# Kernel optimization log

Hardware: AMD Instinct MI355X
Metric: run time of the kernel (lower is better)

## Reference

```python
import jax, jax.numpy as jnp
import numpy as np

N = 100000      # nodes
DIN = 64        # input feature dim
H = 64          # hidden dim
OUT = 2         # classifier output dim
E_REL = 1600000 # edges per relation
E_Q = 1000000   # query edges to classify


def _deg_norm(idx, n, dtype):
    # D^{-1/2} with zero-degree -> 0 (DGL norm='both' semantics)
    deg = jax.ops.segment_sum(jnp.ones(idx.shape[0], dtype=dtype), idx, num_segments=n)
    return jnp.where(deg > 0, jax.lax.rsqrt(jnp.maximum(deg, 1.0)), 0.0)


def graph_conv(x, src, dst, W, b):
    # DGL GraphConv, norm='both': out = D_in^{-1/2} A D_out^{-1/2} x W + b
    n = x.shape[0]
    c_src = _deg_norm(src, n, x.dtype)   # out-degree norm on src side
    c_dst = _deg_norm(dst, n, x.dtype)   # in-degree norm on dst side
    h = x * c_src[:, None]
    agg = jax.ops.segment_sum(h[src], dst, num_segments=n)  # gather -> scatter-add
    agg = agg * c_dst[:, None]
    return agg @ W + b


def setup_inputs() -> dict:
    key = jax.random.key(0)
    ks = jax.random.split(key, 16)
    x = jax.random.normal(ks[0], (N, DIN), dtype=jnp.float32)
    src_pos = jax.random.randint(ks[1], (E_REL,), 0, N)
    dst_pos = jax.random.randint(ks[2], (E_REL,), 0, N)
    src_neg = jax.random.randint(ks[3], (E_REL,), 0, N)
    dst_neg = jax.random.randint(ks[4], (E_REL,), 0, N)
    edge_index = jax.random.randint(ks[5], (2, E_Q), 0, N)
    s_in = 1.0 / np.sqrt(DIN)
    s_h = 1.0 / np.sqrt(H)
    return {
        "x": x,
        "W0_pos": jax.random.uniform(ks[6], (DIN, H), jnp.float32, -s_in, s_in),
        "b0_pos": jnp.zeros((H,), jnp.float32),
        "W0_neg": jax.random.uniform(ks[7], (DIN, H), jnp.float32, -s_in, s_in),
        "b0_neg": jnp.zeros((H,), jnp.float32),
        "W1_pos": jax.random.uniform(ks[8], (H, H), jnp.float32, -s_h, s_h),
        "b1_pos": jnp.zeros((H,), jnp.float32),
        "W1_neg": jax.random.uniform(ks[9], (H, H), jnp.float32, -s_h, s_h),
        "b1_neg": jnp.zeros((H,), jnp.float32),
        "Wc": jax.random.uniform(ks[10], (2 * H, OUT), jnp.float32, -s_h, s_h),
        "bc": jnp.zeros((OUT,), jnp.float32),
        "src_pos": src_pos, "dst_pos": dst_pos,
        "src_neg": src_neg, "dst_neg": dst_neg,
        "edge_index": edge_index,
    }


def reference(x, W0_pos, b0_pos, W0_neg, b0_neg, W1_pos, b1_pos, W1_neg, b1_neg,
              Wc, bc, src_pos, dst_pos, src_neg, dst_neg, edge_index):
    # Layer 1: per-relation GraphConv on input feats, ReLU (HeteroGraphConv 'all' keeps per-relation streams)
    h_pos = jax.nn.relu(graph_conv(x, src_pos, dst_pos, W0_pos, b0_pos))
    h_neg = jax.nn.relu(graph_conv(x, src_neg, dst_neg, W0_neg, b0_neg))
    # Layer 2: each relation stream convolved on its own relation graph
    z_pos = jax.nn.relu(graph_conv(h_pos, src_pos, dst_pos, W1_pos, b1_pos))
    z_neg = jax.nn.relu(graph_conv(h_neg, src_neg, dst_neg, W1_neg, b1_neg))
    z = z_pos - z_neg                         # [N, H]
    src_ids, dst_ids = edge_index[0], edge_index[1]
    h_pair = jnp.concatenate([z[src_ids], z[dst_ids]], axis=1)  # [E_Q, 2H]
    logits = h_pair @ Wc + bc
    return z, jax.nn.sigmoid(logits)
```

## Files before the change

### kernel.cpp

```cpp
#include <hip/hip_runtime.h>
#include <hip/hip_fp16.h>
#include <math.h>

#define N_NODES 100000
#define DIM 64
#define E_REL 1600000
#define E_QQ 1000000

#define NBUCK 196
#define BCAP 9216
#define CHUNK_E 8192
#define P1_BLOCKS ((E_REL + CHUNK_E - 1) / CHUNK_E)

__global__ __launch_bounds__(256) void bin_edges(
    const int* __restrict__ src, const int* __restrict__ dst,
    int* __restrict__ gcur_d, int* __restrict__ gcur_s,
    unsigned* __restrict__ bin_d, unsigned* __restrict__ bin_s) {
  __shared__ int cd[NBUCK];
  __shared__ int cs[NBUCK];
  int t = threadIdx.x;
  for (int i = t; i < NBUCK; i += 256) { cd[i] = 0; cs[i] = 0; }
  __syncthreads();
  int e0 = blockIdx.x * CHUNK_E;
  int e1 = e0 + CHUNK_E;
  if (e1 > E_REL) e1 = E_REL;
  for (int e = e0 + t; e < e1; e += 256) {
    atomicAdd(&cd[dst[e] >> 9], 1);
    atomicAdd(&cs[src[e] >> 9], 1);
  }
  __syncthreads();
  for (int i = t; i < NBUCK; i += 256) {
    cd[i] = atomicAdd(&gcur_d[i], cd[i]);
    cs[i] = atomicAdd(&gcur_s[i], cs[i]);
  }
  __syncthreads();
  for (int e = e0 + t; e < e1; e += 256) {
    int s = src[e];
    int d = dst[e];
    int bd = d >> 9;
    int bs = s >> 9;
    int pd = atomicAdd(&cd[bd], 1);
    int ps = atomicAdd(&cs[bs], 1);
    if ((unsigned)pd < BCAP)
      bin_d[(size_t)bd * BCAP + pd] = (unsigned)(((d & 511) << 17) | s);
    if ((unsigned)ps < BCAP)
      bin_s[(size_t)bs * BCAP + ps] = (unsigned)s;
  }
}

__global__ __launch_bounds__(256) void build_tables(
    const unsigned* __restrict__ bin_d, const int* __restrict__ gcur_d,
    const unsigned* __restrict__ bin_s, const int* __restrict__ gcur_s,
    int* __restrict__ offs, int* __restrict__ degv, int* __restrict__ srclist,
    float* __restrict__ csrc) {
  __shared__ int cnt[512];
  __shared__ int off0[512];
  __shared__ int curv[512];
  __shared__ int ls[256];
  int t = threadIdx.x;
  if (blockIdx.x >= NBUCK) {
    int b = blockIdx.x - NBUCK;
    cnt[t] = 0;
    cnt[t + 256] = 0;
    __syncthreads();
    int n = gcur_s[b];
    if (n > BCAP) n = BCAP;
    const unsigned* be = bin_s + (size_t)b * BCAP;
    for (int i = t; i < n; i += 256) atomicAdd(&cnt[be[i] & 511], 1);
    __syncthreads();
    int node0 = b << 9;
    for (int i = t; i < 512; i += 256) {
      int node = node0 + i;
      if (node < N_NODES) {
        int d = cnt[i];
        csrc[node] = d > 0 ? rsqrtf((float)d) : 0.0f;
      }
    }
    return;
  }
  int b = blockIdx.x;
  cnt[t] = 0;
  cnt[t + 256] = 0;
  __syncthreads();
  int n = gcur_d[b];
  if (n > BCAP) n = BCAP;
  const unsigned* be = bin_d + (size_t)b * BCAP;
  for (int i = t; i < n; i += 256) atomicAdd(&cnt[be[i] >> 17], 1);
  __syncthreads();
  int c0 = cnt[2 * t], c1 = cnt[2 * t + 1];
  ls[t] = c0 + c1;
  __syncthreads();
  for (int off = 1; off < 256; off <<= 1) {
    int v = (t >= off) ? ls[t - off] : 0;
    __syncthreads();
    ls[t] += v;
    __syncthreads();
  }
  int base = ls[t] - (c0 + c1);
  off0[2 * t] = base;
  off0[2 * t + 1] = base + c0;
  curv[2 * t] = base;
  curv[2 * t + 1] = base + c0;
  __syncthreads();
  for (int i = t; i < n; i += 256) {
    unsigned p = be[i];
    int dl = p >> 17;
    int pos = atomicAdd(&curv[dl], 1);
    srclist[(size_t)b * BCAP + pos] = (int)(p & 0x1FFFF);
  }
  __syncthreads();
  int node0 = b << 9;
  for (int i = t; i < 512; i += 256) {
    int node = node0 + i;
    if (node < N_NODES) {
      offs[node] = b * BCAP + off0[i];
      degv[node] = cnt[i];
    }
  }
}

__device__ inline unsigned pack_h2(float a, float b) {
  __half2 h = __floats2half2_rn(a, b);
  return *reinterpret_cast<unsigned*>(&h);
}

__global__ __launch_bounds__(256) void gemm_in_h(
    const float* __restrict__ X, const float* __restrict__ W,
    const float* __restrict__ csrc, __half* __restrict__ Y) {
  __shared__ float Ws[64 * 64];
  for (int t = threadIdx.x; t < 64 * 64; t += 256) Ws[t] = W[t];
  __syncthreads();
  int row = blockIdx.x * 256 + threadIdx.x;
  if (row >= N_NODES) return;
  const float4* xr = (const float4*)(X + (size_t)row * 64);
  float acc[64];
#pragma unroll
  for (int j = 0; j < 64; j++) acc[j] = 0.0f;
#pragma unroll
  for (int k4 = 0; k4 < 16; k4++) {
    float4 xv = xr[k4];
    const float* w0 = &Ws[(k4 * 4 + 0) * 64];
    const float* w1 = &Ws[(k4 * 4 + 1) * 64];
    const float* w2 = &Ws[(k4 * 4 + 2) * 64];
    const float* w3 = &Ws[(k4 * 4 + 3) * 64];
#pragma unroll
    for (int j = 0; j < 64; j++)
      acc[j] += xv.x * w0[j] + xv.y * w1[j] + xv.z * w2[j] + xv.w * w3[j];
  }
  float s = csrc[row];
  uint4* yr = (uint4*)(Y + (size_t)row * 64);
#pragma unroll
  for (int j8 = 0; j8 < 8; j8++) {
    uint4 u;
    u.x = pack_h2(s * acc[j8 * 8 + 0], s * acc[j8 * 8 + 1]);
    u.y = pack_h2(s * acc[j8 * 8 + 2], s * acc[j8 * 8 + 3]);
    u.z = pack_h2(s * acc[j8 * 8 + 4], s * acc[j8 * 8 + 5]);
    u.w = pack_h2(s * acc[j8 * 8 + 6], s * acc[j8 * 8 + 7]);
    yr[j8] = u;
  }
}

__device__ inline float4 agg_quad(const __half* __restrict__ Y, int beg,
                                  int deg, const int* __restrict__ srclist,
                                  int lane, int l, int q) {
  float4 a0 = make_float4(0.f, 0.f, 0.f, 0.f);
  float4 a1 = make_float4(0.f, 0.f, 0.f, 0.f);
  const __half* Yl = Y + 4 * l;
  for (int base = 0; base < deg; base += 64) {
    int chunk = deg - base;
    if (chunk > 64) chunk = 64;
    int sv = (base + lane < deg) ? srclist[beg + base + lane] : 0;
    int nq8 = chunk & ~7;
    for (int j = 0; j < nq8; j += 8) {
      int s0 = __shfl(sv, j + q);
      int s1 = __shfl(sv, j + 4 + q);
      uint2 u0 = *(const uint2*)(Yl + (size_t)s0 * 64);
      uint2 u1 = *(const uint2*)(Yl + (size_t)s1 * 64);
      float2 f;
      f = __half22float2(*reinterpret_cast<__half2*>(&u0.x));
      a0.x += f.x; a0.y += f.y;
      f = __half22float2(*reinterpret_cast<__half2*>(&u0.y));
      a0.z += f.x; a0.w += f.y;
      f = __half22float2(*reinterpret_cast<__half2*>(&u1.x));
      a1.x += f.x; a1.y += f.y;
      f = __half22float2(*reinterpret_cast<__half2*>(&u1.y));
      a1.z += f.x; a1.w += f.y;
    }
    int j0 = nq8 + q;
    int j1 = nq8 + 4 + q;
    int s0 = __shfl(sv, j0 & 63);
    int s1 = __shfl(sv, j1 & 63);
    if (j0 < chunk) {
      uint2 u = *(const uint2*)(Yl + (size_t)s0 * 64);
      float2 f;
      f = __half22float2(*reinterpret_cast<__half2*>(&u.x));
      a0.x += f.x; a0.y += f.y;
      f = __half22float2(*reinterpret_cast<__half2*>(&u.y));
      a0.z += f.x; a0.w += f.y;
    }
    if (j1 < chunk) {
      uint2 u = *(const uint2*)(Yl + (size_t)s1 * 64);
      float2 f;
      f = __half22float2(*reinterpret_cast<__half2*>(&u.x));
      a1.x += f.x; a1.y += f.y;
      f = __half22float2(*reinterpret_cast<__half2*>(&u.y));
      a1.z += f.x; a1.w += f.y;
    }
  }
  a0.x += a1.x; a0.y += a1.y; a0.z += a1.z; a0.w += a1.w;
  a0.x += __shfl_xor(a0.x, 16); a0.y += __shfl_xor(a0.y, 16);
  a0.z += __shfl_xor(a0.z, 16); a0.w += __shfl_xor(a0.w, 16);
  a0.x += __shfl_xor(a0.x, 32); a0.y += __shfl_xor(a0.y, 32);
  a0.z += __shfl_xor(a0.z, 32); a0.w += __shfl_xor(a0.w, 32);
  return a0;
}

__global__ __launch_bounds__(256) void gather_mid(
    const __half* __restrict__ Y, const int* __restrict__ offs,
    const int* __restrict__ degv, const int* __restrict__ srclist,
    const float* __restrict__ b0, const float* __restrict__ csrc,
    const float* __restrict__ W1, __half* __restrict__ Y2) {
  __shared__ float Ws[64 * 64];
  __shared__ float hs[4][64];
  for (int t = threadIdx.x; t < 64 * 64; t += 256) Ws[t] = W1[t];
  __syncthreads();
  int wid = (blockIdx.x * 256 + threadIdx.x) >> 6;
  int lane = threadIdx.x & 63;
  int wslot = threadIdx.x >> 6;
  if (wid >= N_NODES) return;
  int l = lane & 15, q = lane >> 4;
  int beg = offs[wid];
  int deg = degv[wid];
  float4 acc = agg_quad(Y, beg, deg, srclist, lane, l, q);
  float cd = deg > 0 ? rsqrtf((float)deg) : 0.0f;
  float4 bv = ((const float4*)b0)[l];
  float4 h;
  h.x = fmaxf(acc.x * cd + bv.x, 0.0f);
  h.y = fmaxf(acc.y * cd + bv.y, 0.0f);
  h.z = fmaxf(acc.z * cd + bv.z, 0.0f);
  h.w = fmaxf(acc.w * cd + bv.w, 0.0f);
  if (lane < 16) *((float4*)&hs[wslot][4 * l]) = h;
  float acc2 = 0.0f;
#pragma unroll
  for (int k4 = 0; k4 < 16; k4++) {
    float4 hv = *((const float4*)&hs[wslot][4 * k4]);
    acc2 += hv.x * Ws[(4 * k4 + 0) * 64 + lane] +
            hv.y * Ws[(4 * k4 + 1) * 64 + lane] +
            hv.z * Ws[(4 * k4 + 2) * 64 + lane] +
            hv.w * Ws[(4 * k4 + 3) * 64 + lane];
  }
  Y2[(size_t)wid * 64 + lane] = __float2half(csrc[wid] * acc2);
}

template <int MODE>
__global__ __launch_bounds__(256) void gather_fin(
    const __half* __restrict__ Y2, const int* __restrict__ offs,
    const int* __restrict__ degv, const int* __restrict__ srclist,
    const float* __restrict__ b1, float* __restrict__ z,
    float* __restrict__ uv, const float* __restrict__ Wc) {
  __shared__ float Wcs[256];
  if (MODE == 1) {
    Wcs[threadIdx.x] = Wc[threadIdx.x];
    __syncthreads();
  }
  int wid = (blockIdx.x * 256 + threadIdx.x) >> 6;
  int lane = threadIdx.x & 63;
  if (wid >= N_NODES) return;
  int l = lane & 15, q = lane >> 4;
  int beg = offs[wid];
  int deg = degv[wid];
  float4 acc = agg_quad(Y2, beg, deg, srclist, lane, l, q);
  float cd = deg > 0 ? rsqrtf((float)deg) : 0.0f;
  float4 bv = ((const float4*)b1)[l];
  float4 v;
  v.x = fmaxf(acc.x * cd + bv.x, 0.0f);
  v.y = fmaxf(acc.y * cd + bv.y, 0.0f);
  v.z = fmaxf(acc.z * cd + bv.z, 0.0f);
  v.w = fmaxf(acc.w * cd + bv.w, 0.0f);
  float* zrow = z + (size_t)wid * 64 + 4 * l;
  if (MODE == 0) {
    if (lane < 16) *((float4*)zrow) = v;
  } else {
    float4 zo = *((const float4*)zrow);
    float4 r;
    r.x = zo.x - v.x; r.y = zo.y - v.y; r.z = zo.z - v.z; r.w = zo.w - v.w;
    if (lane < 16) *((float4*)zrow) = r;
    float pu0 = r.x * Wcs[(4 * l + 0) * 2 + 0] + r.y * Wcs[(4 * l + 1) * 2 + 0] +
                r.z * Wcs[(4 * l + 2) * 2 + 0] + r.w * Wcs[(4 * l + 3) * 2 + 0];
    float pu1 = r.x * Wcs[(4 * l + 0) * 2 + 1] + r.y * Wcs[(4 * l + 1) * 2 + 1] +
                r.z * Wcs[(4 * l + 2) * 2 + 1] + r.w * Wcs[(4 * l + 3) * 2 + 1];
    float pv0 = r.x * Wcs[(64 + 4 * l + 0) * 2 + 0] + r.y * Wcs[(64 + 4 * l + 1) * 2 + 0] +
                r.z * Wcs[(64 + 4 * l + 2) * 2 + 0] + r.w * Wcs[(64 + 4 * l + 3) * 2 + 0];
    float pv1 = r.x * Wcs[(64 + 4 * l + 0) * 2 + 1] + r.y * Wcs[(64 + 4 * l + 1) * 2 + 1] +
                r.z * Wcs[(64 + 4 * l + 2) * 2 + 1] + r.w * Wcs[(64 + 4 * l + 3) * 2 + 1];
#pragma unroll
    for (int o = 1; o < 16; o <<= 1) {
      pu0 += __shfl_xor(pu0, o);
      pu1 += __shfl_xor(pu1, o);
      pv0 += __shfl_xor(pv0, o);
      pv1 += __shfl_xor(pv1, o);
    }
    if (lane == 0) {
      float4 o4 = make_float4(pu0, pu1, pv0, pv1);
      *((float4*)(uv + (size_t)wid * 4)) = o4;
    }
  }
}

__global__ __launch_bounds__(256) void classify_kernel(
    const float* __restrict__ uv, const int* __restrict__ ei,
    const float* __restrict__ bc, float* __restrict__ out) {
  int e = blockIdx.x * 256 + threadIdx.x;
  if (e >= E_QQ) return;
  int s = ei[e];
  int d = ei[E_QQ + e];
  float4 us = *((const float4*)(uv + (size_t)s * 4));
  float4 vd = *((const float4*)(uv + (size_t)d * 4));
  float l0 = us.x + vd.z + bc[0];
  float l1 = us.y + vd.w + bc[1];
  float2 o;
  o.x = 1.0f / (1.0f + __expf(-l0));
  o.y = 1.0f / (1.0f + __expf(-l1));
  *((float2*)(out + (size_t)e * 2)) = o;
}

extern "C" void kernel_launch(void* const* d_in, const int* in_sizes, int n_in,
                              void* d_out, int out_size, void* d_ws,
                              size_t ws_size, hipStream_t stream) {
  const float* x   = (const float*)d_in[0];
  const float* W0p = (const float*)d_in[1];
  const float* b0p = (const float*)d_in[2];
  const float* W0n = (const float*)d_in[3];
  const float* b0n = (const float*)d_in[4];
  const float* W1p = (const float*)d_in[5];
  const float* b1p = (const float*)d_in[6];
  const float* W1n = (const float*)d_in[7];
  const float* b1n = (const float*)d_in[8];
  const float* Wc  = (const float*)d_in[9];
  const float* bc  = (const float*)d_in[10];
  const int* sp = (const int*)d_in[11];
  const int* dp = (const int*)d_in[12];
  const int* sn = (const int*)d_in[13];
  const int* dn = (const int*)d_in[14];
  const int* ei = (const int*)d_in[15];

  float* csrc_p = (float*)d_ws;
  float* csrc_n = csrc_p + N_NODES;
  int* offs_p = (int*)(csrc_n + N_NODES);
  int* deg_p  = offs_p + N_NODES;
  int* offs_n = deg_p + N_NODES;
  int* deg_n  = offs_n + N_NODES;
  float* uv   = (float*)(deg_n + N_NODES);
  int* gcur   = (int*)(uv + 4 * N_NODES);
  unsigned* bin_d = (unsigned*)(gcur + 2 * NBUCK + 2);
  unsigned* bin_s = bin_d + (size_t)NBUCK * BCAP;
  int* srclist = (int*)(bin_s + (size_t)NBUCK * BCAP);
  __half* A = (__half*)(srclist + (size_t)NBUCK * BCAP);
  __half* B = A + (size_t)N_NODES * 64;

  float* z     = (float*)d_out;
  float* probs = z + (size_t)N_NODES * 64;

  int* gcur_d = gcur;
  int* gcur_s = gcur + NBUCK;

  const int gemmGrid = (N_NODES + 255) / 256;
  const int aggGrid  = (N_NODES * 64 + 255) / 256;

  hipMemsetAsync(gcur, 0, 2 * NBUCK * sizeof(int), stream);
  bin_edges<<<P1_BLOCKS, 256, 0, stream>>>(sp, dp, gcur_d, gcur_s, bin_d, bin_s);
  build_tables<<<2 * NBUCK, 256, 0, stream>>>(bin_d, gcur_d, bin_s, gcur_s,
                                              offs_p, deg_p, srclist, csrc_p);
  gemm_in_h<<<gemmGrid, 256, 0, stream>>>(x, W0p, csrc_p, A);
  gather_mid<<<aggGrid, 256, 0, stream>>>(A, offs_p, deg_p, srclist, b0p,
                                          csrc_p, W1p, B);
  gather_fin<0><<<aggGrid, 256, 0, stream>>>(B, offs_p, deg_p, srclist, b1p, z,
                                             uv, Wc);

  hipMemsetAsync(gcur, 0, 2 * NBUCK * sizeof(int), stream);
  bin_edges<<<P1_BLOCKS, 256, 0, stream>>>(sn, dn, gcur_d, gcur_s, bin_d, bin_s);
  build_tables<<<2 * NBUCK, 256, 0, stream>>>(bin_d, gcur_d, bin_s, gcur_s,
                                              offs_n, deg_n, srclist, csrc_n);
  gemm_in_h<<<gemmGrid, 256, 0, stream>>>(x, W0n, csrc_n, A);
  gather_mid<<<aggGrid, 256, 0, stream>>>(A, offs_n, deg_n, srclist, b0n,
                                          csrc_n, W1n, B);
  gather_fin<1><<<aggGrid, 256, 0, stream>>>(B, offs_n, deg_n, srclist, b1n, z,
                                             uv, Wc);

  classify_kernel<<<(E_QQ + 255) / 256, 256, 0, stream>>>(uv, ei, bc, probs);
}
```

Measured before the change: 627.7 us.

## Split features into 16-wide column planes and gather per plane with persistent blocks

Feature matrices are stored as four column-chunk planes of 16 halfs each, and the gather runs once per plane so each plane's working set (about 3.2 MB) stays cache-resident during the random-access gathers. The mid-layer matmul is pulled out of the gather into its own kernel, and the final uv projection moves into a separate kernel. This cuts cache misses on random row gathers, at the cost of re-reading the srclist four times and adding extra kernel launches and an extra pass over intermediate tensors.

```diff
diff --git a/kernel.cpp b/kernel.cpp
--- a/kernel.cpp
+++ b/kernel.cpp
@@ -11,6 +11,9 @@
 #define BCAP 9216
 #define CHUNK_E 8192
 #define P1_BLOCKS ((E_REL + CHUNK_E - 1) / CHUNK_E)
+#define NBLK_N 1563
+#define NCH 16
+#define N16 ((size_t)N_NODES * NCH)
 
 __global__ __launch_bounds__(256) void bin_edges(
     const int* __restrict__ src, const int* __restrict__ dst,
@@ -148,163 +151,167 @@
       acc[j] += xv.x * w0[j] + xv.y * w1[j] + xv.z * w2[j] + xv.w * w3[j];
   }
   float s = csrc[row];
-  uint4* yr = (uint4*)(Y + (size_t)row * 64);
-#pragma unroll
-  for (int j8 = 0; j8 < 8; j8++) {
-    uint4 u;
-    u.x = pack_h2(s * acc[j8 * 8 + 0], s * acc[j8 * 8 + 1]);
-    u.y = pack_h2(s * acc[j8 * 8 + 2], s * acc[j8 * 8 + 3]);
-    u.z = pack_h2(s * acc[j8 * 8 + 4], s * acc[j8 * 8 + 5]);
-    u.w = pack_h2(s * acc[j8 * 8 + 6], s * acc[j8 * 8 + 7]);
-    yr[j8] = u;
-  }
-}
-
-__device__ inline float4 agg_quad(const __half* __restrict__ Y, int beg,
-                                  int deg, const int* __restrict__ srclist,
-                                  int lane, int l, int q) {
-  float4 a0 = make_float4(0.f, 0.f, 0.f, 0.f);
-  float4 a1 = make_float4(0.f, 0.f, 0.f, 0.f);
-  const __half* Yl = Y + 4 * l;
-  for (int base = 0; base < deg; base += 64) {
-    int chunk = deg - base;
-    if (chunk > 64) chunk = 64;
-    int sv = (base + lane < deg) ? srclist[beg + base + lane] : 0;
-    int nq8 = chunk & ~7;
-    for (int j = 0; j < nq8; j += 8) {
-      int s0 = __shfl(sv, j + q);
-      int s1 = __shfl(sv, j + 4 + q);
-      uint2 u0 = *(const uint2*)(Yl + (size_t)s0 * 64);
-      uint2 u1 = *(const uint2*)(Yl + (size_t)s1 * 64);
-      float2 f;
-      f = __half22float2(*reinterpret_cast<__half2*>(&u0.x));
-      a0.x += f.x; a0.y += f.y;
-      f = __half22float2(*reinterpret_cast<__half2*>(&u0.y));
-      a0.z += f.x; a0.w += f.y;
-      f = __half22float2(*reinterpret_cast<__half2*>(&u1.x));
-      a1.x += f.x; a1.y += f.y;
-      f = __half22float2(*reinterpret_cast<__half2*>(&u1.y));
-      a1.z += f.x; a1.w += f.y;
-    }
-    int j0 = nq8 + q;
-    int j1 = nq8 + 4 + q;
-    int s0 = __shfl(sv, j0 & 63);
-    int s1 = __shfl(sv, j1 & 63);
-    if (j0 < chunk) {
-      uint2 u = *(const uint2*)(Yl + (size_t)s0 * 64);
-      float2 f;
-      f = __half22float2(*reinterpret_cast<__half2*>(&u.x));
-      a0.x += f.x; a0.y += f.y;
-      f = __half22float2(*reinterpret_cast<__half2*>(&u.y));
-      a0.z += f.x; a0.w += f.y;
-    }
-    if (j1 < chunk) {
-      uint2 u = *(const uint2*)(Yl + (size_t)s1 * 64);
-      float2 f;
-      f = __half22float2(*reinterpret_cast<__half2*>(&u.x));
-      a1.x += f.x; a1.y += f.y;
-      f = __half22float2(*reinterpret_cast<__half2*>(&u.y));
-      a1.z += f.x; a1.w += f.y;
-    }
-  }
-  a0.x += a1.x; a0.y += a1.y; a0.z += a1.z; a0.w += a1.w;
-  a0.x += __shfl_xor(a0.x, 16); a0.y += __shfl_xor(a0.y, 16);
-  a0.z += __shfl_xor(a0.z, 16); a0.w += __shfl_xor(a0.w, 16);
-  a0.x += __shfl_xor(a0.x, 32); a0.y += __shfl_xor(a0.y, 32);
-  a0.z += __shfl_xor(a0.z, 32); a0.w += __shfl_xor(a0.w, 32);
-  return a0;
-}
-
-__global__ __launch_bounds__(256) void gather_mid(
-    const __half* __restrict__ Y, const int* __restrict__ offs,
+#pragma unroll
+  for (int c = 0; c < 4; c++) {
+    uint4* yc = (uint4*)(Y + (size_t)c * N16 + (size_t)row * NCH);
+#pragma unroll
+    for (int h = 0; h < 2; h++) {
+      int f = c * 16 + h * 8;
+      uint4 u;
+      u.x = pack_h2(s * acc[f + 0], s * acc[f + 1]);
+      u.y = pack_h2(s * acc[f + 2], s * acc[f + 3]);
+      u.z = pack_h2(s * acc[f + 4], s * acc[f + 5]);
+      u.w = pack_h2(s * acc[f + 6], s * acc[f + 7]);
+      yc[h] = u;
+    }
+  }
+}
+
+__global__ __launch_bounds__(256) void gemm_mid_h(
+    const __half* __restrict__ X, const float* __restrict__ W,
+    const float* __restrict__ csrc, __half* __restrict__ Y) {
+  __shared__ float Ws[64 * 64];
+  for (int t = threadIdx.x; t < 64 * 64; t += 256) Ws[t] = W[t];
+  __syncthreads();
+  int row = blockIdx.x * 256 + threadIdx.x;
+  if (row >= N_NODES) return;
+  float acc[64];
+#pragma unroll
+  for (int j = 0; j < 64; j++) acc[j] = 0.0f;
+#pragma unroll
+  for (int c = 0; c < 4; c++) {
+    const uint4* xr = (const uint4*)(X + (size_t)c * N16 + (size_t)row * NCH);
+#pragma unroll
+    for (int h = 0; h < 2; h++) {
+      uint4 u = xr[h];
+      float2 f0 = __half22float2(*(__half2*)&u.x);
+      float2 f1 = __half22float2(*(__half2*)&u.y);
+      float2 f2 = __half22float2(*(__half2*)&u.z);
+      float2 f3 = __half22float2(*(__half2*)&u.w);
+      const float* w = &Ws[(c * 16 + h * 8) * 64];
+#pragma unroll
+      for (int j = 0; j < 64; j++)
+        acc[j] += f0.x * w[0 * 64 + j] + f0.y * w[1 * 64 + j] +
+                  f1.x * w[2 * 64 + j] + f1.y * w[3 * 64 + j] +
+                  f2.x * w[4 * 64 + j] + f2.y * w[5 * 64 + j] +
+                  f3.x * w[6 * 64 + j] + f3.y * w[7 * 64 + j];
+    }
+  }
+  float s = csrc[row];
+#pragma unroll
+  for (int c = 0; c < 4; c++) {
+    uint4* yc = (uint4*)(Y + (size_t)c * N16 + (size_t)row * NCH);
+#pragma unroll
+    for (int h = 0; h < 2; h++) {
+      int f = c * 16 + h * 8;
+      uint4 u;
+      u.x = pack_h2(s * acc[f + 0], s * acc[f + 1]);
+      u.y = pack_h2(s * acc[f + 2], s * acc[f + 3]);
+      u.z = pack_h2(s * acc[f + 4], s * acc[f + 5]);
+      u.w = pack_h2(s * acc[f + 6], s * acc[f + 7]);
+      yc[h] = u;
+    }
+  }
+}
+
+template <int PHASE>
+__global__ __launch_bounds__(256) void gather_split(
+    const __half* __restrict__ Yc, const int* __restrict__ offs,
     const int* __restrict__ degv, const int* __restrict__ srclist,
-    const float* __restrict__ b0, const float* __restrict__ csrc,
-    const float* __restrict__ W1, __half* __restrict__ Y2) {
-  __shared__ float Ws[64 * 64];
-  __shared__ float hs[4][64];
-  for (int t = threadIdx.x; t < 64 * 64; t += 256) Ws[t] = W1[t];
-  __syncthreads();
-  int wid = (blockIdx.x * 256 + threadIdx.x) >> 6;
+    const float* __restrict__ bias, __half* __restrict__ Hout,
+    float* __restrict__ z) {
+  int p = blockIdx.x / NBLK_N;
+  int nb = blockIdx.x - p * NBLK_N;
   int lane = threadIdx.x & 63;
   int wslot = threadIdx.x >> 6;
-  if (wid >= N_NODES) return;
-  int l = lane & 15, q = lane >> 4;
-  int beg = offs[wid];
-  int deg = degv[wid];
-  float4 acc = agg_quad(Y, beg, deg, srclist, lane, l, q);
-  float cd = deg > 0 ? rsqrtf((float)deg) : 0.0f;
-  float4 bv = ((const float4*)b0)[l];
-  float4 h;
-  h.x = fmaxf(acc.x * cd + bv.x, 0.0f);
-  h.y = fmaxf(acc.y * cd + bv.y, 0.0f);
-  h.z = fmaxf(acc.z * cd + bv.z, 0.0f);
-  h.w = fmaxf(acc.w * cd + bv.w, 0.0f);
-  if (lane < 16) *((float4*)&hs[wslot][4 * l]) = h;
-  float acc2 = 0.0f;
-#pragma unroll
-  for (int k4 = 0; k4 < 16; k4++) {
-    float4 hv = *((const float4*)&hs[wslot][4 * k4]);
-    acc2 += hv.x * Ws[(4 * k4 + 0) * 64 + lane] +
-            hv.y * Ws[(4 * k4 + 1) * 64 + lane] +
-            hv.z * Ws[(4 * k4 + 2) * 64 + lane] +
-            hv.w * Ws[(4 * k4 + 3) * 64 + lane];
-  }
-  Y2[(size_t)wid * 64 + lane] = __float2half(csrc[wid] * acc2);
-}
-
-template <int MODE>
-__global__ __launch_bounds__(256) void gather_fin(
-    const __half* __restrict__ Y2, const int* __restrict__ offs,
-    const int* __restrict__ degv, const int* __restrict__ srclist,
-    const float* __restrict__ b1, float* __restrict__ z,
-    float* __restrict__ uv, const float* __restrict__ Wc) {
-  __shared__ float Wcs[256];
-  if (MODE == 1) {
-    Wcs[threadIdx.x] = Wc[threadIdx.x];
-    __syncthreads();
-  }
+  int g = lane >> 2;
+  int c = lane & 3;
+  const __half* Yp = Yc + (size_t)p * N16 + 4 * c;
+  float4 bv = ((const float4*)bias)[p * 4 + c];
+  for (int wid = nb * 4 + wslot; wid < N_NODES; wid += NBLK_N * 4) {
+    int beg = offs[wid];
+    int deg = degv[wid];
+    float4 a0 = make_float4(0.f, 0.f, 0.f, 0.f);
+    float4 a1 = make_float4(0.f, 0.f, 0.f, 0.f);
+    for (int base = 0; base < deg; base += 64) {
+      int chunk = deg - base;
+      if (chunk > 64) chunk = 64;
+      int sv = (base + lane < deg) ? srclist[beg + base + lane] : 0;
+      for (int k = 0; k < chunk; k += 32) {
+        int j0 = k + g;
+        int j1 = k + 16 + g;
+        int s0 = __shfl(sv, j0 & 63);
+        int s1 = __shfl(sv, j1 & 63);
+        if (j0 < chunk) {
+          uint2 u = *(const uint2*)(Yp + (size_t)s0 * NCH);
+          float2 f0 = __half22float2(*(__half2*)&u.x);
+          float2 f1 = __half22float2(*(__half2*)&u.y);
+          a0.x += f0.x; a0.y += f0.y; a0.z += f1.x; a0.w += f1.y;
+        }
+        if (j1 < chunk) {
+          uint2 u = *(const uint2*)(Yp + (size_t)s1 * NCH);
+          float2 f0 = __half22float2(*(__half2*)&u.x);
+          float2 f1 = __half22float2(*(__half2*)&u.y);
+          a1.x += f0.x; a1.y += f0.y; a1.z += f1.x; a1.w += f1.y;
+        }
+      }
+    }
+    a0.x += a1.x; a0.y += a1.y; a0.z += a1.z; a0.w += a1.w;
+#pragma unroll
+    for (int o = 4; o < 64; o <<= 1) {
+      a0.x += __shfl_xor(a0.x, o);
+      a0.y += __shfl_xor(a0.y, o);
+      a0.z += __shfl_xor(a0.z, o);
+      a0.w += __shfl_xor(a0.w, o);
+    }
+    float cd = deg > 0 ? rsqrtf((float)deg) : 0.0f;
+    float4 v;
+    v.x = fmaxf(a0.x * cd + bv.x, 0.0f);
+    v.y = fmaxf(a0.y * cd + bv.y, 0.0f);
+    v.z = fmaxf(a0.z * cd + bv.z, 0.0f);
+    v.w = fmaxf(a0.w * cd + bv.w, 0.0f);
+    if (PHASE == 0) {
+      if (g == 0) {
+        uint2 u;
+        u.x = pack_h2(v.x, v.y);
+        u.y = pack_h2(v.z, v.w);
+        *(uint2*)(Hout + (size_t)p * N16 + (size_t)wid * NCH + 4 * c) = u;
+      }
+    } else if (PHASE == 1) {
+      if (g == 0)
+        *(float4*)(z + (size_t)wid * 64 + p * 16 + 4 * c) = v;
+    } else {
+      if (g == 0) {
+        float4* zp = (float4*)(z + (size_t)wid * 64 + p * 16 + 4 * c);
+        float4 zo = *zp;
+        zo.x -= v.x; zo.y -= v.y; zo.z -= v.z; zo.w -= v.w;
+        *zp = zo;
+      }
+    }
+  }
+}
+
+__global__ __launch_bounds__(256) void uv_kernel(
+    const float* __restrict__ z, const float* __restrict__ Wc,
+    float* __restrict__ uv) {
   int wid = (blockIdx.x * 256 + threadIdx.x) >> 6;
   int lane = threadIdx.x & 63;
   if (wid >= N_NODES) return;
-  int l = lane & 15, q = lane >> 4;
-  int beg = offs[wid];
-  int deg = degv[wid];
-  float4 acc = agg_quad(Y2, beg, deg, srclist, lane, l, q);
-  float cd = deg > 0 ? rsqrtf((float)deg) : 0.0f;
-  float4 bv = ((const float4*)b1)[l];
-  float4 v;
-  v.x = fmaxf(acc.x * cd + bv.x, 0.0f);
-  v.y = fmaxf(acc.y * cd + bv.y, 0.0f);
-  v.z = fmaxf(acc.z * cd + bv.z, 0.0f);
-  v.w = fmaxf(acc.w * cd + bv.w, 0.0f);
-  float* zrow = z + (size_t)wid * 64 + 4 * l;
-  if (MODE == 0) {
-    if (lane < 16) *((float4*)zrow) = v;
-  } else {
-    float4 zo = *((const float4*)zrow);
-    float4 r;
-    r.x = zo.x - v.x; r.y = zo.y - v.y; r.z = zo.z - v.z; r.w = zo.w - v.w;
-    if (lane < 16) *((float4*)zrow) = r;
-    float pu0 = r.x * Wcs[(4 * l + 0) * 2 + 0] + r.y * Wcs[(4 * l + 1) * 2 + 0] +
-                r.z * Wcs[(4 * l + 2) * 2 + 0] + r.w * Wcs[(4 * l + 3) * 2 + 0];
-    float pu1 = r.x * Wcs[(4 * l + 0) * 2 + 1] + r.y * Wcs[(4 * l + 1) * 2 + 1] +
-                r.z * Wcs[(4 * l + 2) * 2 + 1] + r.w * Wcs[(4 * l + 3) * 2 + 1];
-    float pv0 = r.x * Wcs[(64 + 4 * l + 0) * 2 + 0] + r.y * Wcs[(64 + 4 * l + 1) * 2 + 0] +
-                r.z * Wcs[(64 + 4 * l + 2) * 2 + 0] + r.w * Wcs[(64 + 4 * l + 3) * 2 + 0];
-    float pv1 = r.x * Wcs[(64 + 4 * l + 0) * 2 + 1] + r.y * Wcs[(64 + 4 * l + 1) * 2 + 1] +
-                r.z * Wcs[(64 + 4 * l + 2) * 2 + 1] + r.w * Wcs[(64 + 4 * l + 3) * 2 + 1];
-#pragma unroll
-    for (int o = 1; o < 16; o <<= 1) {
-      pu0 += __shfl_xor(pu0, o);
-      pu1 += __shfl_xor(pu1, o);
-      pv0 += __shfl_xor(pv0, o);
-      pv1 += __shfl_xor(pv1, o);
-    }
-    if (lane == 0) {
-      float4 o4 = make_float4(pu0, pu1, pv0, pv1);
-      *((float4*)(uv + (size_t)wid * 4)) = o4;
-    }
-  }
+  float w0 = Wc[lane * 2 + 0];
+  float w1 = Wc[lane * 2 + 1];
+  float w2 = Wc[(64 + lane) * 2 + 0];
+  float w3 = Wc[(64 + lane) * 2 + 1];
+  float r = z[(size_t)wid * 64 + lane];
+  float p0 = r * w0, p1 = r * w1, p2 = r * w2, p3 = r * w3;
+#pragma unroll
+  for (int o = 1; o < 64; o <<= 1) {
+    p0 += __shfl_xor(p0, o);
+    p1 += __shfl_xor(p1, o);
+    p2 += __shfl_xor(p2, o);
+    p3 += __shfl_xor(p3, o);
+  }
+  if (lane == 0)
+    *(float4*)(uv + (size_t)wid * 4) = make_float4(p0, p1, p2, p3);
 }
 
 __global__ __launch_bounds__(256) void classify_kernel(
@@ -344,14 +351,11 @@
   const int* dn = (const int*)d_in[14];
   const int* ei = (const int*)d_in[15];
 
-  float* csrc_p = (float*)d_ws;
-  float* csrc_n = csrc_p + N_NODES;
-  int* offs_p = (int*)(csrc_n + N_NODES);
-  int* deg_p  = offs_p + N_NODES;
-  int* offs_n = deg_p + N_NODES;
-  int* deg_n  = offs_n + N_NODES;
-  float* uv   = (float*)(deg_n + N_NODES);
-  int* gcur   = (int*)(uv + 4 * N_NODES);
+  float* csrc = (float*)d_ws;
+  int* degv = (int*)(csrc + N_NODES);
+  int* offs = degv + N_NODES;
+  float* uv = (float*)(offs + N_NODES);
+  int* gcur = (int*)(uv + 4 * N_NODES);
   unsigned* bin_d = (unsigned*)(gcur + 2 * NBUCK + 2);
   unsigned* bin_s = bin_d + (size_t)NBUCK * BCAP;
   int* srclist = (int*)(bin_s + (size_t)NBUCK * BCAP);
@@ -365,27 +369,30 @@
   int* gcur_s = gcur + NBUCK;
 
   const int gemmGrid = (N_NODES + 255) / 256;
-  const int aggGrid  = (N_NODES * 64 + 255) / 256;
+  const int gathGrid = 4 * NBLK_N;
 
   hipMemsetAsync(gcur, 0, 2 * NBUCK * sizeof(int), stream);
   bin_edges<<<P1_BLOCKS, 256, 0, stream>>>(sp, dp, gcur_d, gcur_s, bin_d, bin_s);
   build_tables<<<2 * NBUCK, 256, 0, stream>>>(bin_d, gcur_d, bin_s, gcur_s,
-                                              offs_p, deg_p, srclist, csrc_p);
-  gemm_in_h<<<gemmGrid, 256, 0, stream>>>(x, W0p, csrc_p, A);
-  gather_mid<<<aggGrid, 256, 0, stream>>>(A, offs_p, deg_p, srclist, b0p,
-                                          csrc_p, W1p, B);
-  gather_fin<0><<<aggGrid, 256, 0, stream>>>(B, offs_p, deg_p, srclist, b1p, z,
-                                             uv, Wc);
+                                              offs, degv, srclist, csrc);
+  gemm_in_h<<<gemmGrid, 256, 0, stream>>>(x, W0p, csrc, A);
+  gather_split<0><<<gathGrid, 256, 0, stream>>>(A, offs, degv, srclist, b0p, B,
+                                                nullptr);
+  gemm_mid_h<<<gemmGrid, 256, 0, stream>>>(B, W1p, csrc, A);
+  gather_split<1><<<gathGrid, 256, 0, stream>>>(A, offs, degv, srclist, b1p,
+                                                nullptr, z);
 
   hipMemsetAsync(gcur, 0, 2 * NBUCK * sizeof(int), stream);
   bin_edges<<<P1_BLOCKS, 256, 0, stream>>>(sn, dn, gcur_d, gcur_s, bin_d, bin_s);
   build_tables<<<2 * NBUCK, 256, 0, stream>>>(bin_d, gcur_d, bin_s, gcur_s,
-                                              offs_n, deg_n, srclist, csrc_n);
-  gemm_in_h<<<gemmGrid, 256, 0, stream>>>(x, W0n, csrc_n, A);
-  gather_mid<<<aggGrid, 256, 0, stream>>>(A, offs_n, deg_n, srclist, b0n,
-                                          csrc_n, W1n, B);
-  gather_fin<1><<<aggGrid, 256, 0, stream>>>(B, offs_n, deg_n, srclist, b1n, z,
-                                             uv, Wc);
-
+                                              offs, degv, srclist, csrc);
+  gemm_in_h<<<gemmGrid, 256, 0, stream>>>(x, W0n, csrc, A);
+  gather_split<0><<<gathGrid, 256, 0, stream>>>(A, offs, degv, srclist, b0n, B,
+                                                nullptr);
+  gemm_mid_h<<<gemmGrid, 256, 0, stream>>>(B, W1n, csrc, A);
+  gather_split<2><<<gathGrid, 256, 0, stream>>>(A, offs, degv, srclist, b1n,
+                                                nullptr, z);
+
+  uv_kernel<<<(N_NODES * 64 + 255) / 256, 256, 0, stream>>>(z, Wc, uv);
   classify_kernel<<<(E_QQ + 255) / 256, 256, 0, stream>>>(uv, ei, bc, probs);
 }
```

New measurement: 902.9 us. +43.8%, slower.
